# Kernel optimization log

Measured on AMD Instinct MI355X. Metric: run time of the kernel, lower is better.

Reference implementation:

```python
import jax, jax.numpy as jnp
import numpy as np

N_SUB = 32      # n_subgraphs
SIZE = 10       # size_subgraph
MAX_STEP = 4
N_GRAPHS = 128
EPS = 1e-5      # BatchNorm eps


def setup_inputs() -> dict:
    key = jax.random.key(0)
    ks = jax.random.split(key, 4)
    n_nodes = 2048
    # sparse-valued symmetric adjacency, avg degree ~16
    p = 16.0 / n_nodes
    u = jax.random.uniform(ks[0], (n_nodes, n_nodes))
    upper = jnp.triu((u < p).astype(jnp.float32), k=1)
    adj = upper + upper.T
    # sorted balanced graph assignment: every graph id in [0,128) appears (16 nodes each)
    graph_indicator = ((jnp.arange(n_nodes) * N_GRAPHS) // n_nodes).astype(jnp.int32)
    n_pairs = SIZE * (SIZE - 1) // 2  # 45
    theta = jax.random.normal(ks[1], (N_SUB, n_pairs, 1), dtype=jnp.float32) * np.float32(np.sqrt(2.0 / n_pairs))
    feat = N_SUB * (MAX_STEP - 1)  # 96
    hidden, out_dim = 128, 2
    gamma = jnp.ones((feat,), jnp.float32)
    beta = jnp.zeros((feat,), jnp.float32)
    w1 = jax.random.normal(ks[2], (feat, hidden), dtype=jnp.float32) * 0.1
    b1 = jnp.zeros((hidden,), jnp.float32)
    w2 = jax.random.normal(ks[3], (hidden, out_dim), dtype=jnp.float32) * 0.1
    b2 = jnp.zeros((out_dim,), jnp.float32)
    return dict(adj=adj, graph_indicator=graph_indicator, theta=theta,
                gamma=gamma, beta=beta, w1=w1, b1=b1, w2=w2, b2=b2)


def reference(adj, graph_indicator, theta, gamma, beta, w1, b1, w2, b2):
    n_nodes = adj.shape[0]
    # learned hidden subgraphs: relu(Theta) scattered into symmetric [S, k, k]
    sampled = jax.nn.relu(theta[:, :, 0])                      # [S, k(k-1)/2]
    iu = jnp.triu_indices(SIZE, k=1)
    a_sub = jnp.zeros((N_SUB, SIZE, SIZE), adj.dtype).at[:, iu[0], iu[1]].set(sampled)
    a_sub = a_sub + jnp.swapaxes(a_sub, 1, 2)                  # [S, k, k]
    # per-graph node counts (all graphs present by construction)
    counts = jax.ops.segment_sum(jnp.ones((n_nodes,), adj.dtype), graph_indicator,
                                 num_segments=N_GRAPHS)        # [G]
    adj_pow = jnp.eye(n_nodes, dtype=adj.dtype)                # torch's I, becomes adj^i
    p_pow = jnp.ones((N_SUB, SIZE, n_nodes), adj.dtype)        # torch's P_power_E (E is all ones)
    feats = []
    for _ in range(1, MAX_STEP):
        adj_pow = adj @ adj_pow                                # adj^i  [N, N]
        p_pow = jnp.einsum('skt,stn->skn', a_sub, p_pow)       # A_sub^i @ E
        res = jnp.einsum('skn,nm->skm', p_pow, adj_pow)        # [S, k, N] (mul by E==ones is a no-op)
        # scatter-sum over nodes into graphs, then sum over subgraph-node axis k
        pooled = jax.ops.segment_sum(jnp.moveaxis(res, 2, 0), graph_indicator,
                                     num_segments=N_GRAPHS)    # [G, S, k]
        r = pooled.sum(axis=2)                                 # [G, S]
        r = r / counts[:, None]                                # normalize=True
        feats.append(r)
    x = jnp.concatenate(feats, axis=1)                         # [G, S*(max_step-1)]
    # BatchNorm1d, training mode (biased batch stats)
    mean = x.mean(axis=0)
    var = x.var(axis=0)
    x = gamma * (x - mean) * jax.lax.rsqrt(var + EPS) + beta
    h = jax.nn.relu(x @ w1 + b1)
    return h @ w2 + b2                                         # [G, output_dim]
```

## Files before the change

### kernel.cpp

```cpp
#include <hip/hip_runtime.h>
#include <math.h>

#define N_NODES  2048
#define N_GRAPHS 128
#define NSUB     32
#define SSZ      10
#define NPAIRS   45
#define FEAT     96
#define HIDDEN   128
#define BN_EPS   1e-5f

#define MAXD     128

#define WS_C1   0
#define WS_DEG  2048
#define WS_CG1  4096
#define WS_CG2  4224
#define WS_CG3  4352
#define WS_EDG  4608

__device__ __forceinline__ float aload(const float* p) {
    return __hip_atomic_load(const_cast<float*>(p), __ATOMIC_RELAXED, __HIP_MEMORY_SCOPE_AGENT);
}
__device__ __forceinline__ void afadd(float* p, float v) {
    __hip_atomic_fetch_add(p, v, __ATOMIC_RELAXED, __HIP_MEMORY_SCOPE_AGENT);
}

__global__ __launch_bounds__(256) void k_build(const float* __restrict__ A,
                                               float* __restrict__ ws) {
    __shared__ int nnzc[4];
    const int wv   = threadIdx.x >> 6;
    const int lane = threadIdx.x & 63;
    const int row  = (blockIdx.x << 2) + wv;
    const float* Ar = A + (size_t)row * N_NODES;
    float* c1  = ws + WS_C1;
    int*  degp = (int*)(ws + WS_DEG);
    int2* ep   = (int2*)(ws + WS_EDG) + (size_t)row * MAXD;

    if (blockIdx.x == 0 && threadIdx.x < 384) ws[WS_CG1 + threadIdx.x] = 0.f;

    if (lane == 0) nnzc[wv] = 0;
    __syncthreads();

    float s = 0.f;
    for (int c = lane * 4; c < N_NODES; c += 256) {
        float4 a = *reinterpret_cast<const float4*>(Ar + c);
        s += (a.x + a.y) + (a.z + a.w);
        if (a.x != 0.f) { int p = atomicAdd(&nnzc[wv], 1); if (p < MAXD) ep[p] = make_int2(c,     __float_as_int(a.x)); }
        if (a.y != 0.f) { int p = atomicAdd(&nnzc[wv], 1); if (p < MAXD) ep[p] = make_int2(c + 1, __float_as_int(a.y)); }
        if (a.z != 0.f) { int p = atomicAdd(&nnzc[wv], 1); if (p < MAXD) ep[p] = make_int2(c + 2, __float_as_int(a.z)); }
        if (a.w != 0.f) { int p = atomicAdd(&nnzc[wv], 1); if (p < MAXD) ep[p] = make_int2(c + 3, __float_as_int(a.w)); }
    }
    #pragma unroll
    for (int o = 32; o; o >>= 1) s += __shfl_down(s, o);
    __syncthreads();
    if (lane == 0) { c1[row] = s; degp[row] = nnzc[wv]; }
}

__global__ __launch_bounds__(256) void k_hop(const float* __restrict__ ws_ro,
                                             float* __restrict__ ws_rw,
                                             const int* __restrict__ gi) {
    const int wv   = threadIdx.x >> 6;
    const int lane = threadIdx.x & 63;
    const int row  = (blockIdx.x << 2) + wv;

    const float* c1   = ws_ro + WS_C1;
    const int*   degp = (const int*)(ws_ro + WS_DEG);
    const int2*  edg  = (const int2*)(ws_ro + WS_EDG);
    const int2*  ep   = edg + (size_t)row * MAXD;

    const int nz = min(degp[row], MAXD);

    float acc2 = 0.f;
    for (int k = lane; k < nz; k += 64) {
        int2 e = ep[k];
        acc2 = fmaf(__int_as_float(e.y), c1[e.x], acc2);
    }

    const int sub = lane & 3, grp = lane >> 2;
    float acc3 = 0.f;
    for (int base = 0; base < nz; base += 16) {
        const int k = base + grp;
        float contrib = 0.f;
        if (k < nz) {
            int2 e = ep[k];
            const int   j   = e.x;
            const float arj = __int_as_float(e.y);
            const int   dj  = min(degp[j], MAXD);
            const int2* epj = edg + (size_t)j * MAXD;
            float pj = 0.f;
            for (int m = sub; m < dj; m += 4) {
                int2 ej = epj[m];
                pj = fmaf(__int_as_float(ej.y), c1[ej.x], pj);
            }
            pj += __shfl_xor(pj, 1);
            pj += __shfl_xor(pj, 2);
            if (sub == 0) contrib = arj * pj;
        }
        acc3 += contrib;
    }

    #pragma unroll
    for (int o = 32; o; o >>= 1) { acc2 += __shfl_down(acc2, o); acc3 += __shfl_down(acc3, o); }

    if (lane == 0) {
        const int g = gi[row];
        afadd(ws_rw + WS_CG1 + g, c1[row]);
        afadd(ws_rw + WS_CG2 + g, acc2);
        afadd(ws_rw + WS_CG3 + g, acc3);
    }
}

__global__ __launch_bounds__(256)
void k_tail(const int*   __restrict__ gi,
            const float* __restrict__ ws_ro,
            const float* __restrict__ theta,
            const float* __restrict__ gamma,
            const float* __restrict__ beta,
            const float* __restrict__ w1,
            const float* __restrict__ b1,
            const float* __restrict__ w2,
            const float* __restrict__ b2,
            float* __restrict__ out) {
    __shared__ float cnt_s[N_GRAPHS];
    __shared__ float Vl[3][NSUB];
    __shared__ float yl[3][N_GRAPHS];
    __shared__ float mv[6];
    __shared__ float xr[FEAT];
    __shared__ float red[4];

    const int tid  = threadIdx.x;
    const int wv   = tid >> 6;
    const int lane = tid & 63;
    const int g    = blockIdx.x;

    if (tid < N_GRAPHS) cnt_s[tid] = 0.f;
    __syncthreads();
    for (int n = tid; n < N_NODES; n += 256) atomicAdd(&cnt_s[gi[n]], 1.f);

    if (tid < NSUB) {
        const float* th = theta + tid * NPAIRS;
        float u1[SSZ];
        #pragma unroll
        for (int k = 0; k < SSZ; k++) u1[k] = 0.f;
        float sumT = 0.f;
        #pragma unroll
        for (int i = 0; i < SSZ; i++) {
            #pragma unroll
            for (int j = i + 1; j < SSZ; j++) {
                const int p = i * (2 * SSZ - 1 - i) / 2 + (j - i - 1);
                float t = th[p]; t = t > 0.f ? t : 0.f;
                sumT += t; u1[i] += t; u1[j] += t;
            }
        }
        float V2 = 0.f;
        #pragma unroll
        for (int k = 0; k < SSZ; k++) V2 += u1[k] * u1[k];
        float V3 = 0.f;
        #pragma unroll
        for (int i = 0; i < SSZ; i++) {
            #pragma unroll
            for (int j = i + 1; j < SSZ; j++) {
                const int p = i * (2 * SSZ - 1 - i) / 2 + (j - i - 1);
                float t = th[p]; t = t > 0.f ? t : 0.f;
                V3 += t * u1[i] * u1[j];
            }
        }
        Vl[0][tid] = 2.f * sumT;
        Vl[1][tid] = V2;
        Vl[2][tid] = 2.f * V3;
    }
    __syncthreads();

    if (tid < N_GRAPHS) {
        float inv = 1.f / cnt_s[tid];
        yl[0][tid] = aload(ws_ro + WS_CG1 + tid) * inv;
        yl[1][tid] = aload(ws_ro + WS_CG2 + tid) * inv;
        yl[2][tid] = aload(ws_ro + WS_CG3 + tid) * inv;
    }
    __syncthreads();

    if (wv < 3) {
        float a = yl[wv][lane], b = yl[wv][lane + 64];
        float s = a + b;
        #pragma unroll
        for (int o = 32; o; o >>= 1) s += __shfl_xor(s, o);
        float m = s * (1.f / N_GRAPHS);
        float da = a - m, db = b - m;
        float v = da * da + db * db;
        #pragma unroll
        for (int o = 32; o; o >>= 1) v += __shfl_xor(v, o);
        v *= (1.f / N_GRAPHS);
        if (lane == 0) { mv[wv] = m; mv[3 + wv] = v; }
    }
    __syncthreads();

    if (tid < FEAT) {
        int i = tid >> 5;
        float V = Vl[i][tid & 31];
        float scale = gamma[tid] * rsqrtf(V * V * mv[3 + i] + BN_EPS);
        xr[tid] = scale * V * (yl[i][g] - mv[i]) + beta[tid];
    }
    __syncthreads();

    if (tid < HIDDEN) {
        float acc = b1[tid];
        #pragma unroll
        for (int f = 0; f < FEAT; f++)
            acc = fmaf(xr[f], w1[f * HIDDEN + tid], acc);
        float h = fmaxf(acc, 0.f);
        float2 w2v = *reinterpret_cast<const float2*>(w2 + 2 * tid);
        float p0 = h * w2v.x, p1 = h * w2v.y;
        #pragma unroll
        for (int o = 32; o; o >>= 1) { p0 += __shfl_down(p0, o); p1 += __shfl_down(p1, o); }
        int w = tid >> 6, l = tid & 63;
        if (l == 0) { red[2 * w] = p0; red[2 * w + 1] = p1; }
    }
    __syncthreads();
    if (tid == 0) {
        out[2 * g + 0] = red[0] + red[2] + b2[0];
        out[2 * g + 1] = red[1] + red[3] + b2[1];
    }
}

extern "C" void kernel_launch(void* const* d_in, const int* in_sizes, int n_in,
                              void* d_out, int out_size, void* d_ws, size_t ws_size,
                              hipStream_t stream) {
    const float* adj   = (const float*)d_in[0];
    const int*   gi    = (const int*)  d_in[1];
    const float* theta = (const float*)d_in[2];
    const float* gamma = (const float*)d_in[3];
    const float* beta  = (const float*)d_in[4];
    const float* w1    = (const float*)d_in[5];
    const float* b1    = (const float*)d_in[6];
    const float* w2    = (const float*)d_in[7];
    const float* b2    = (const float*)d_in[8];
    float* out = (float*)d_out;
    float* ws  = (float*)d_ws;

    k_build<<<512, 256, 0, stream>>>(adj, ws);
    k_hop  <<<512, 256, 0, stream>>>(ws, ws, gi);
    k_tail <<<N_GRAPHS, 256, 0, stream>>>(gi, ws, theta, gamma, beta,
                                          w1, b1, w2, b2, out);
}
```

Baseline: 28.75 us.

## Fuse hop and tail kernels via a grid-wide spin barrier

Merges the two-hop propagation kernel and the batchnorm/MLP tail into one kernel of 128 blocks. Each block processes 16 rows and then synchronises with the others through a flag/generation spin barrier in the workspace. Per-graph node counts are now accumulated with global atomics instead of being recomputed in every tail block. This removes one kernel launch and the redundant count pass, but there is less parallelism in the hop phase (128 blocks instead of 512). The barrier also depends on all blocks being co-resident, and the flags are cleared each call by the build kernel.

```diff
diff --git a/kernel.cpp b/kernel.cpp
--- a/kernel.cpp
+++ b/kernel.cpp
@@ -11,16 +11,28 @@
 #define BN_EPS   1e-5f
 
 #define MAXD     128
+#define NBLK_R   128
+#define RPB_R    16
 
 #define WS_C1   0
 #define WS_DEG  2048
 #define WS_CG1  4096
 #define WS_CG2  4224
 #define WS_CG3  4352
-#define WS_EDG  4608
+#define WS_CNT  4480
+#define WS_FLG  4608
+#define WS_GEN  4736
+#define WS_EDG  4744
+#define WS_ZN   648
 
 __device__ __forceinline__ float aload(const float* p) {
     return __hip_atomic_load(const_cast<float*>(p), __ATOMIC_RELAXED, __HIP_MEMORY_SCOPE_AGENT);
+}
+__device__ __forceinline__ int aiload(int* p) {
+    return __hip_atomic_load(p, __ATOMIC_RELAXED, __HIP_MEMORY_SCOPE_AGENT);
+}
+__device__ __forceinline__ void aistore(int* p, int v) {
+    __hip_atomic_store(p, v, __ATOMIC_RELAXED, __HIP_MEMORY_SCOPE_AGENT);
 }
 __device__ __forceinline__ void afadd(float* p, float v) {
     __hip_atomic_fetch_add(p, v, __ATOMIC_RELAXED, __HIP_MEMORY_SCOPE_AGENT);
@@ -37,7 +49,8 @@
     int*  degp = (int*)(ws + WS_DEG);
     int2* ep   = (int2*)(ws + WS_EDG) + (size_t)row * MAXD;
 
-    if (blockIdx.x == 0 && threadIdx.x < 384) ws[WS_CG1 + threadIdx.x] = 0.f;
+    if (blockIdx.x == 0)
+        for (int i = threadIdx.x; i < WS_ZN; i += 256) ws[WS_CG1 + i] = 0.f;
 
     if (lane == 0) nnzc[wv] = 0;
     __syncthreads();
@@ -57,63 +70,9 @@
     if (lane == 0) { c1[row] = s; degp[row] = nnzc[wv]; }
 }
 
-__global__ __launch_bounds__(256) void k_hop(const float* __restrict__ ws_ro,
-                                             float* __restrict__ ws_rw,
-                                             const int* __restrict__ gi) {
-    const int wv   = threadIdx.x >> 6;
-    const int lane = threadIdx.x & 63;
-    const int row  = (blockIdx.x << 2) + wv;
-
-    const float* c1   = ws_ro + WS_C1;
-    const int*   degp = (const int*)(ws_ro + WS_DEG);
-    const int2*  edg  = (const int2*)(ws_ro + WS_EDG);
-    const int2*  ep   = edg + (size_t)row * MAXD;
-
-    const int nz = min(degp[row], MAXD);
-
-    float acc2 = 0.f;
-    for (int k = lane; k < nz; k += 64) {
-        int2 e = ep[k];
-        acc2 = fmaf(__int_as_float(e.y), c1[e.x], acc2);
-    }
-
-    const int sub = lane & 3, grp = lane >> 2;
-    float acc3 = 0.f;
-    for (int base = 0; base < nz; base += 16) {
-        const int k = base + grp;
-        float contrib = 0.f;
-        if (k < nz) {
-            int2 e = ep[k];
-            const int   j   = e.x;
-            const float arj = __int_as_float(e.y);
-            const int   dj  = min(degp[j], MAXD);
-            const int2* epj = edg + (size_t)j * MAXD;
-            float pj = 0.f;
-            for (int m = sub; m < dj; m += 4) {
-                int2 ej = epj[m];
-                pj = fmaf(__int_as_float(ej.y), c1[ej.x], pj);
-            }
-            pj += __shfl_xor(pj, 1);
-            pj += __shfl_xor(pj, 2);
-            if (sub == 0) contrib = arj * pj;
-        }
-        acc3 += contrib;
-    }
-
-    #pragma unroll
-    for (int o = 32; o; o >>= 1) { acc2 += __shfl_down(acc2, o); acc3 += __shfl_down(acc3, o); }
-
-    if (lane == 0) {
-        const int g = gi[row];
-        afadd(ws_rw + WS_CG1 + g, c1[row]);
-        afadd(ws_rw + WS_CG2 + g, acc2);
-        afadd(ws_rw + WS_CG3 + g, acc3);
-    }
-}
-
 __global__ __launch_bounds__(256)
-void k_tail(const int*   __restrict__ gi,
-            const float* __restrict__ ws_ro,
+void k_rest(float* __restrict__ ws,
+            const int*   __restrict__ gi,
             const float* __restrict__ theta,
             const float* __restrict__ gamma,
             const float* __restrict__ beta,
@@ -122,7 +81,6 @@
             const float* __restrict__ w2,
             const float* __restrict__ b2,
             float* __restrict__ out) {
-    __shared__ float cnt_s[N_GRAPHS];
     __shared__ float Vl[3][NSUB];
     __shared__ float yl[3][N_GRAPHS];
     __shared__ float mv[6];
@@ -132,11 +90,72 @@
     const int tid  = threadIdx.x;
     const int wv   = tid >> 6;
     const int lane = tid & 63;
-    const int g    = blockIdx.x;
-
-    if (tid < N_GRAPHS) cnt_s[tid] = 0.f;
-    __syncthreads();
-    for (int n = tid; n < N_NODES; n += 256) atomicAdd(&cnt_s[gi[n]], 1.f);
+    const int bid  = blockIdx.x;
+
+    const float* c1   = ws + WS_C1;
+    const int*   degp = (const int*)(ws + WS_DEG);
+    const int2*  edg  = (const int2*)(ws + WS_EDG);
+    int* flags = (int*)(ws + WS_FLG);
+    int* gen   = (int*)(ws + WS_GEN);
+
+    #pragma unroll
+    for (int r = 0; r < 4; r++) {
+        const int row = bid * RPB_R + wv * 4 + r;
+        const int2* ep = edg + (size_t)row * MAXD;
+        const int nz = min(degp[row], MAXD);
+
+        float acc2 = 0.f;
+        for (int k = lane; k < nz; k += 64) {
+            int2 e = ep[k];
+            acc2 = fmaf(__int_as_float(e.y), c1[e.x], acc2);
+        }
+        const int sub = lane & 3, grp = lane >> 2;
+        float acc3 = 0.f;
+        for (int base = 0; base < nz; base += 16) {
+            const int k = base + grp;
+            float contrib = 0.f;
+            if (k < nz) {
+                int2 e = ep[k];
+                const int   j   = e.x;
+                const float arj = __int_as_float(e.y);
+                const int   dj  = min(degp[j], MAXD);
+                const int2* epj = edg + (size_t)j * MAXD;
+                float pj = 0.f;
+                for (int m = sub; m < dj; m += 4) {
+                    int2 ej = epj[m];
+                    pj = fmaf(__int_as_float(ej.y), c1[ej.x], pj);
+                }
+                pj += __shfl_xor(pj, 1);
+                pj += __shfl_xor(pj, 2);
+                if (sub == 0) contrib = arj * pj;
+            }
+            acc3 += contrib;
+        }
+        #pragma unroll
+        for (int o = 32; o; o >>= 1) { acc2 += __shfl_down(acc2, o); acc3 += __shfl_down(acc3, o); }
+        if (lane == 0) {
+            const int g = gi[row];
+            afadd(ws + WS_CG1 + g, c1[row]);
+            afadd(ws + WS_CG2 + g, acc2);
+            afadd(ws + WS_CG3 + g, acc3);
+            afadd(ws + WS_CNT + g, 1.f);
+        }
+    }
+
+    __syncthreads();
+    if (tid == 0) aistore(flags + bid, 1);
+    if (bid == 0) {
+        if (tid < NBLK_R)
+            while (aiload(flags + tid) == 0) __builtin_amdgcn_s_sleep(1);
+        __syncthreads();
+        if (tid == 0) aistore(gen, 1);
+    } else {
+        if (tid == 0)
+            while (aiload(gen) == 0) __builtin_amdgcn_s_sleep(1);
+        __syncthreads();
+    }
+
+    const int g = bid;
 
     if (tid < NSUB) {
         const float* th = theta + tid * NPAIRS;
@@ -170,13 +189,12 @@
         Vl[1][tid] = V2;
         Vl[2][tid] = 2.f * V3;
     }
-    __syncthreads();
 
     if (tid < N_GRAPHS) {
-        float inv = 1.f / cnt_s[tid];
-        yl[0][tid] = aload(ws_ro + WS_CG1 + tid) * inv;
-        yl[1][tid] = aload(ws_ro + WS_CG2 + tid) * inv;
-        yl[2][tid] = aload(ws_ro + WS_CG3 + tid) * inv;
+        float inv = 1.f / aload(ws + WS_CNT + tid);
+        yl[0][tid] = aload(ws + WS_CG1 + tid) * inv;
+        yl[1][tid] = aload(ws + WS_CG2 + tid) * inv;
+        yl[2][tid] = aload(ws + WS_CG3 + tid) * inv;
     }
     __syncthreads();
 
@@ -239,7 +257,6 @@
     float* ws  = (float*)d_ws;
 
     k_build<<<512, 256, 0, stream>>>(adj, ws);
-    k_hop  <<<512, 256, 0, stream>>>(ws, ws, gi);
-    k_tail <<<N_GRAPHS, 256, 0, stream>>>(gi, ws, theta, gamma, beta,
-                                          w1, b1, w2, b2, out);
-}
+    k_rest <<<NBLK_R, 256, 0, stream>>>(ws, gi, theta, gamma, beta,
+                                        w1, b1, w2, b2, out);
+}
```

After: 35.40 us. 1.23x slower.
